# Kernel optimization log

Hardware: AMD Instinct MI355X
Metric: run time of the kernel (lower is better)

Reference implementation:

```python
import jax, jax.numpy as jnp
import numpy as np


def setup_inputs() -> dict:
    key = jax.random.key(0)
    ks = jax.random.split(key, 6)
    B, C, H, W = 4, 256, 64, 64
    C8 = C // 8
    s = 0.05
    return {
        "x": jax.random.normal(ks[0], (B, C, H, W), dtype=jnp.float32),
        "Wf": jax.random.normal(ks[1], (C8, C), dtype=jnp.float32) * s,
        "bf": jnp.zeros((C8,), dtype=jnp.float32),
        "Wg": jax.random.normal(ks[2], (C8, C), dtype=jnp.float32) * s,
        "bg": jnp.zeros((C8,), dtype=jnp.float32),
        "Wh": jax.random.normal(ks[3], (C, C), dtype=jnp.float32) * s,
        "bh": jnp.zeros((C,), dtype=jnp.float32),
        "gamma": jnp.ones((1,), dtype=jnp.float32),
    }


def reference(x, Wf, bf, Wg, bg, Wh, bh, gamma):
    B, C, H, W = x.shape
    N = H * W
    xf = x.reshape(B, C, N)  # [B, C, N] (1x1 conv == matmul over channels)
    f = jnp.einsum("kc,bcn->bkn", Wf, xf) + bf[None, :, None]  # [B, C/8, N]
    g = jnp.einsum("kc,bcn->bkn", Wg, xf) + bg[None, :, None]  # [B, C/8, N]
    h = jnp.einsum("oc,bcn->bon", Wh, xf) + bh[None, :, None]  # [B, C, N]
    # attention_map[b, n, m] = sum_k f[b,k,n] * g[b,k,m]  (f^T g)
    attn = jnp.einsum("bkn,bkm->bnm", f, g)  # [B, N, N]
    # softmax over dim -2 (the f-position axis), as in the torch module
    attn = jax.nn.softmax(attn, axis=-2)
    # out[b,c,m] = sum_n h[b,c,n] * attn[b,n,m]
    out = jnp.einsum("bcn,bnm->bcm", h, attn).reshape(B, C, H, W)
    return gamma * out + x
```

## Files before the change

kernel.cpp:

```cpp
#include <hip/hip_runtime.h>
#include <hip/hip_bf16.h>
#include <hip/hip_fp16.h>

typedef __attribute__((ext_vector_type(8))) short short8;
typedef __attribute__((ext_vector_type(8))) _Float16 half8;
typedef __attribute__((ext_vector_type(4))) float f32x4;
typedef unsigned short u16;
typedef unsigned int u32;

#define LOG2E 1.44269504088896f

__device__ __forceinline__ u16 f2bf(float f) {
  u32 u = __builtin_bit_cast(u32, f);
  u += 0x7fffu + ((u >> 16) & 1u);
  return (u16)(u >> 16);
}
__device__ __forceinline__ u16 f2h(float f) {
  _Float16 h = (_Float16)f;
  return __builtin_bit_cast(u16, h);
}

__global__ void k_prep(const float* __restrict__ x,
                       const float* __restrict__ Wf, const float* __restrict__ bfp,
                       const float* __restrict__ Wg, const float* __restrict__ bgp,
                       const float* __restrict__ Wh, const float* __restrict__ bhp,
                       u16* __restrict__ xT, u16* __restrict__ Wall,
                       float* __restrict__ ball)
{
  int bid = blockIdx.x, t = threadIdx.x;
  if (bid < 1024) {
    __shared__ u16 tile[64][68];
    int b = bid >> 8, c0 = ((bid >> 6) & 3) << 6, n0 = (bid & 63) << 6;
#pragma unroll
    for (int r = 0; r < 4; ++r) {
      int cl = (t >> 4) + r * 16, nl = (t & 15) * 4;
      const float4 v = *(const float4*)&x[(size_t)(b * 256 + c0 + cl) * 4096 + n0 + nl];
      tile[cl][nl + 0] = f2h(v.x); tile[cl][nl + 1] = f2h(v.y);
      tile[cl][nl + 2] = f2h(v.z); tile[cl][nl + 3] = f2h(v.w);
    }
    __syncthreads();
#pragma unroll
    for (int r = 0; r < 4; ++r) {
      int nl = (t >> 4) + r * 16, cl = (t & 15) * 4;
      ushort4 o;
      o.x = tile[cl + 0][nl]; o.y = tile[cl + 1][nl];
      o.z = tile[cl + 2][nl]; o.w = tile[cl + 3][nl];
      *(ushort4*)&xT[(size_t)(b * 4096 + n0 + nl) * 256 + c0 + cl] = o;
    }
  } else {
    int wb = bid - 1024;
    int e = wb * 1024 + t * 4;
    int r = e >> 8, c = e & 255;
    const float* src = (r < 32) ? (Wf + r * 256 + c)
                     : (r < 64) ? (Wg + (r - 32) * 256 + c)
                                : (Wh + (r - 64) * 256 + c);
    float4 v = *(const float4*)src;
    ushort4 o; o.x = f2h(v.x); o.y = f2h(v.y); o.z = f2h(v.z); o.w = f2h(v.w);
    *(ushort4*)&Wall[e] = o;
    if (wb == 0 && t < 80) {
#pragma unroll
      for (int i = 0; i < 4; ++i) {
        int idx = t * 4 + i;
        ball[idx] = (idx < 32) ? bfp[idx] : (idx < 64) ? bgp[idx - 32] : bhp[idx - 64];
      }
    }
  }
}

__global__ __launch_bounds__(256, 4)
void k_proj(const u16* __restrict__ xT, const u16* __restrict__ Wall,
            const float* __restrict__ ball,
            u16* __restrict__ q, u16* __restrict__ kmat, u16* __restrict__ hbf)
{
  int bid = blockIdx.x, t = threadIdx.x;
  int w = t >> 6, l = t & 63, lg = l >> 4, li = l & 15;
  f32x4 Z = {0.f, 0.f, 0.f, 0.f};
  if (bid < 256) {
    int b = bid >> 6, n0 = (bid & 63) << 6;
    int rbase = w * 16;
    half8 aw[8];
#pragma unroll
    for (int kk = 0; kk < 8; ++kk)
      aw[kk] = *(const half8*)&Wall[(rbase + li) * 256 + kk * 32 + lg * 8];
    float bias[4];
#pragma unroll
    for (int j = 0; j < 4; ++j) bias[j] = ball[rbase + 4 * lg + j];
#pragma unroll
    for (int nn = 0; nn < 4; ++nn) {
      int n = n0 + nn * 16 + li;
      f32x4 acc = Z;
#pragma unroll
      for (int kk = 0; kk < 8; ++kk) {
        half8 bx = *(const half8*)&xT[(size_t)(b * 4096 + n) * 256 + kk * 32 + lg * 8];
        acc = __builtin_amdgcn_mfma_f32_16x16x32_f16(aw[kk], bx, acc, 0, 0, 0);
      }
      ushort4 o;
      o.x = f2h(acc[0] + bias[0]); o.y = f2h(acc[1] + bias[1]);
      o.z = f2h(acc[2] + bias[2]); o.w = f2h(acc[3] + bias[3]);
      u16* dst = (rbase < 32)
               ? (kmat + (size_t)(b * 4096 + n) * 32 + rbase + 4 * lg)
               : (q    + (size_t)(b * 4096 + n) * 32 + (rbase - 32) + 4 * lg);
      *(ushort4*)dst = o;
    }
  } else {
    int hb = bid - 256;
    int b = hb >> 8, rt = (hb >> 6) & 3, n0 = (hb & 63) << 6;
    int r0 = 64 + rt * 64;
    int nbase = n0 + w * 16;
    half8 ax[8];
#pragma unroll
    for (int kk = 0; kk < 8; ++kk)
      ax[kk] = *(const half8*)&xT[(size_t)(b * 4096 + nbase + li) * 256 + kk * 32 + lg * 8];
#pragma unroll
    for (int rr = 0; rr < 4; ++rr) {
      int r = r0 + rr * 16 + li;
      f32x4 acc = Z;
#pragma unroll
      for (int kk = 0; kk < 8; ++kk) {
        half8 bw = *(const half8*)&Wall[r * 256 + kk * 32 + lg * 8];
        acc = __builtin_amdgcn_mfma_f32_16x16x32_f16(ax[kk], bw, acc, 0, 0, 0);
      }
      float bias = ball[r];
      ushort4 o;
      o.x = f2bf(acc[0] + bias); o.y = f2bf(acc[1] + bias);
      o.z = f2bf(acc[2] + bias); o.w = f2bf(acc[3] + bias);
      *(ushort4*)&hbf[(size_t)(b * 256 + r - 64) * 4096 + nbase + 4 * lg] = o;
    }
  }
}

__global__ __launch_bounds__(512, 2)
void k_attn(const u16* __restrict__ q, const u16* __restrict__ kmat,
            const u16* __restrict__ hbf, const float* __restrict__ xin,
            const float* __restrict__ gam, float* __restrict__ out)
{
  __shared__ __align__(16) u16 Pl[64 * 64];
  __shared__ float mrg[2 * 4096];
  __shared__ float sums[64];

  int bid = blockIdx.x, t = threadIdx.x;
  int b = (bid >> 1) & 3;
  int mt = ((bid >> 3) << 1) | (bid & 1);
  int m0 = mt << 6;
  int w = t >> 6, l = t & 63, lg = l >> 4, li = l & 15;
  int msub = w & 3, nh = w >> 2;
  int csub = msub,  kh = nh;

  const u16* qb = q    + (size_t)b * 4096 * 32;
  const u16* kb = kmat + (size_t)b * 4096 * 32;
  const u16* hb = hbf  + (size_t)b * 256 * 4096;

  half8 aQ = *(const half8*)&qb[(m0 + msub * 16 + li) * 32 + lg * 8];

  f32x4 Z = {0.f, 0.f, 0.f, 0.f};
  f32x4 acc[4][4];
#pragma unroll
  for (int mi = 0; mi < 4; ++mi)
#pragma unroll
    for (int ci = 0; ci < 4; ++ci) acc[mi][ci] = Z;
  float vsum[4] = {0.f, 0.f, 0.f, 0.f};

  half8 kf0 = *(const half8*)&kb[((nh * 2 + 0) * 16 + li) * 32 + lg * 8];
  half8 kf1 = *(const half8*)&kb[((nh * 2 + 1) * 16 + li) * 32 + lg * 8];
  short8 vb[4];
#pragma unroll
  for (int ff = 0; ff < 4; ++ff)
    vb[ff] = *(const short8*)&hb[(size_t)(csub * 64 + ff * 16 + li) * 4096 + kh * 32 + lg * 8];

  for (int it = 0; it < 64; ++it) {
    int n0 = it * 64;
    int n1 = (n0 + 64) & 4095;

    f32x4 s0 = __builtin_amdgcn_mfma_f32_16x16x32_f16(aQ, kf0, Z, 0, 0, 0);
    f32x4 s1 = __builtin_amdgcn_mfma_f32_16x16x32_f16(aQ, kf1, Z, 0, 0, 0);

    kf0 = *(const half8*)&kb[(n1 + (nh * 2 + 0) * 16 + li) * 32 + lg * 8];
    kf1 = *(const half8*)&kb[(n1 + (nh * 2 + 1) * 16 + li) * 32 + lg * 8];

    u16 pu[8];
#pragma unroll
    for (int j = 0; j < 4; ++j) {
      float p0 = exp2f(s0[j] * LOG2E);
      float p1 = exp2f(s1[j] * LOG2E);
      vsum[j] += p0 + p1;
      pu[j]     = f2bf(p0);
      pu[4 + j] = f2bf(p1);
    }

    asm volatile("s_waitcnt lgkmcnt(0)" ::: "memory");
    __builtin_amdgcn_s_barrier();

#pragma unroll
    for (int s = 0; s < 2; ++s) {
      int nc = (nh * 2 + s) * 16 + li;
#pragma unroll
      for (int j = 0; j < 4; ++j) {
        int m = msub * 16 + 4 * lg + j;
        Pl[m * 64 + (((nc >> 3) ^ (m & 7)) << 3) + (nc & 7)] = pu[s * 4 + j];
      }
    }

    asm volatile("s_waitcnt lgkmcnt(0)" ::: "memory");
    __builtin_amdgcn_s_barrier();

    short8 pa[4];
#pragma unroll
    for (int mi = 0; mi < 4; ++mi) {
      int m = mi * 16 + li;
      int blk = (kh * 4 + lg) ^ (m & 7);
      pa[mi] = *(const short8*)&Pl[m * 64 + blk * 8];
    }
#pragma unroll
    for (int mi = 0; mi < 4; ++mi)
#pragma unroll
      for (int ci = 0; ci < 4; ++ci)
        acc[mi][ci] = __builtin_amdgcn_mfma_f32_16x16x32_bf16(pa[mi], vb[ci], acc[mi][ci], 0, 0, 0);

#pragma unroll
    for (int ff = 0; ff < 4; ++ff)
      vb[ff] = *(const short8*)&hb[(size_t)(csub * 64 + ff * 16 + li) * 4096 + n1 + kh * 32 + lg * 8];
  }

#pragma unroll
  for (int j = 0; j < 4; ++j) {
    float v = vsum[j];
    v += __shfl_xor(v, 1); v += __shfl_xor(v, 2);
    v += __shfl_xor(v, 4); v += __shfl_xor(v, 8);
    vsum[j] = v;
  }
  int mrow = msub * 16 + 4 * lg;
  if (nh == 0 && li == 0) {
#pragma unroll
    for (int j = 0; j < 4; ++j) sums[mrow + j] = vsum[j];
  }
  if (w == 4 || w == 5) {
#pragma unroll
    for (int mi = 0; mi < 4; ++mi)
#pragma unroll
      for (int ci = 0; ci < 4; ++ci)
#pragma unroll
        for (int j = 0; j < 4; ++j)
          mrg[(w - 4) * 4096 + (mi * 16 + ci * 4 + j) * 64 + l] = acc[mi][ci][j];
  }
  __syncthreads();
  if (nh == 1 && li == 0) {
#pragma unroll
    for (int j = 0; j < 4; ++j) sums[mrow + j] += vsum[j];
  }
  if (w == 0 || w == 1) {
#pragma unroll
    for (int mi = 0; mi < 4; ++mi)
#pragma unroll
      for (int ci = 0; ci < 4; ++ci)
#pragma unroll
        for (int j = 0; j < 4; ++j)
          acc[mi][ci][j] += mrg[w * 4096 + (mi * 16 + ci * 4 + j) * 64 + l];
  }
  __syncthreads();
  if (t < 64) sums[t] = 1.0f / sums[t];
  if (w == 6 || w == 7) {
#pragma unroll
    for (int mi = 0; mi < 4; ++mi)
#pragma unroll
      for (int ci = 0; ci < 4; ++ci)
#pragma unroll
        for (int j = 0; j < 4; ++j)
          mrg[(w - 6) * 4096 + (mi * 16 + ci * 4 + j) * 64 + l] = acc[mi][ci][j];
  }
  __syncthreads();
  if (w == 2 || w == 3) {
#pragma unroll
    for (int mi = 0; mi < 4; ++mi)
#pragma unroll
      for (int ci = 0; ci < 4; ++ci)
#pragma unroll
        for (int j = 0; j < 4; ++j)
          acc[mi][ci][j] += mrg[(w - 2) * 4096 + (mi * 16 + ci * 4 + j) * 64 + l];
  }
  if (w < 4) {
    float gamma = gam[0];
    float* ob = out + (size_t)b * 256 * 4096;
    const float* xb = xin + (size_t)b * 256 * 4096;
#pragma unroll
    for (int mi = 0; mi < 4; ++mi) {
      float inv[4];
#pragma unroll
      for (int j = 0; j < 4; ++j) inv[j] = sums[mi * 16 + 4 * lg + j];
#pragma unroll
      for (int ci = 0; ci < 4; ++ci) {
        int c = csub * 64 + ci * 16 + li;
        size_t base = (size_t)c * 4096 + m0 + mi * 16 + 4 * lg;
        float4 xv = *(const float4*)&xb[base];
        float4 ov;
        ov.x = gamma * acc[mi][ci][0] * inv[0] + xv.x;
        ov.y = gamma * acc[mi][ci][1] * inv[1] + xv.y;
        ov.z = gamma * acc[mi][ci][2] * inv[2] + xv.z;
        ov.w = gamma * acc[mi][ci][3] * inv[3] + xv.w;
        *(float4*)&ob[base] = ov;
      }
    }
  }
}

extern "C" void kernel_launch(void* const* d_in, const int* in_sizes, int n_in,
                              void* d_out, int out_size, void* d_ws, size_t ws_size,
                              hipStream_t stream)
{
  const float* x   = (const float*)d_in[0];
  const float* Wf  = (const float*)d_in[1];
  const float* bfp = (const float*)d_in[2];
  const float* Wg  = (const float*)d_in[3];
  const float* bgp = (const float*)d_in[4];
  const float* Wh  = (const float*)d_in[5];
  const float* bhp = (const float*)d_in[6];
  const float* gam = (const float*)d_in[7];
  float* out = (float*)d_out;

  char* ws = (char*)d_ws;
  u16*   xT   = (u16*)(ws);
  u16*   Wall = (u16*)(ws + 8388608);
  float* ball = (float*)(ws + 8552448);
  u16*   q    = (u16*)(ws + 8554496);
  u16*   km   = (u16*)(ws + 10651648);
  u16*   hbf  = (u16*)(ws + 12748800);

  k_prep<<<dim3(1104), dim3(256), 0, stream>>>(x, Wf, bfp, Wg, bgp, Wh, bhp, xT, Wall, ball);
  k_proj<<<dim3(1280), dim3(256), 0, stream>>>(xT, Wall, ball, q, km, hbf);
  k_attn<<<dim3(256),  dim3(512), 0, stream>>>(q, km, hbf, x, gam, out);
}
```

Before: 115.3 us.

## Restructure attention kernel with 32x32 MFMA, register-resident P and split-N warps

Rewrites the attention main loop to use 32x32x16 MFMAs, computing S transposed (K as A operand) so each lane's exp'd probabilities feed the PV MFMA directly from registers. This removes the LDS round-trip for P and one of the two barriers per iteration. Warps split the N range in halves with double-buffered K/V register prefetch and s_setprio around the MFMA block. The LOG2E scale is folded into the g weights and bias at prep time, and the final cross-warp reduction is simplified to a single swizzled LDS merge. Larger accumulators and double buffers raise register pressure, and the V loads become narrower 8-byte accesses.

```diff
diff --git a/kernel.cpp b/kernel.cpp
--- a/kernel.cpp
+++ b/kernel.cpp
@@ -5,6 +5,8 @@
 typedef __attribute__((ext_vector_type(8))) short short8;
 typedef __attribute__((ext_vector_type(8))) _Float16 half8;
 typedef __attribute__((ext_vector_type(4))) float f32x4;
+typedef __attribute__((ext_vector_type(16))) float f32x16;
+typedef __attribute__((ext_vector_type(4))) unsigned int uint4v;
 typedef unsigned short u16;
 typedef unsigned int u32;
 
@@ -18,6 +20,11 @@
 __device__ __forceinline__ u16 f2h(float f) {
   _Float16 h = (_Float16)f;
   return __builtin_bit_cast(u16, h);
+}
+__device__ __forceinline__ u32 cvtpk_bf16(float lo, float hi) {
+  u32 r;
+  asm("v_cvt_pk_bf16_f32 %0, %1, %2" : "=v"(r) : "v"(lo), "v"(hi));
+  return r;
 }
 
 __global__ void k_prep(const float* __restrict__ x,
@@ -50,18 +57,23 @@
   } else {
     int wb = bid - 1024;
     int e = wb * 1024 + t * 4;
-    int r = e >> 8, c = e & 255;
-    const float* src = (r < 32) ? (Wf + r * 256 + c)
-                     : (r < 64) ? (Wg + (r - 32) * 256 + c)
-                                : (Wh + (r - 64) * 256 + c);
+    int r = e >> 8;
+    const float* src = (r < 32) ? (Wf + e)
+                     : (r < 64) ? (Wg + e - 32 * 256)
+                                : (Wh + e - 64 * 256);
     float4 v = *(const float4*)src;
-    ushort4 o; o.x = f2h(v.x); o.y = f2h(v.y); o.z = f2h(v.z); o.w = f2h(v.w);
+    float sc = (r >= 32 && r < 64) ? LOG2E : 1.0f;
+    ushort4 o;
+    o.x = f2h(v.x * sc); o.y = f2h(v.y * sc);
+    o.z = f2h(v.z * sc); o.w = f2h(v.w * sc);
     *(ushort4*)&Wall[e] = o;
     if (wb == 0 && t < 80) {
 #pragma unroll
       for (int i = 0; i < 4; ++i) {
         int idx = t * 4 + i;
-        ball[idx] = (idx < 32) ? bfp[idx] : (idx < 64) ? bgp[idx - 32] : bhp[idx - 64];
+        ball[idx] = (idx < 32) ? bfp[idx]
+                  : (idx < 64) ? bgp[idx - 32] * LOG2E
+                               : bhp[idx - 64];
       }
     }
   }
@@ -134,168 +146,144 @@
             const u16* __restrict__ hbf, const float* __restrict__ xin,
             const float* __restrict__ gam, float* __restrict__ out)
 {
-  __shared__ __align__(16) u16 Pl[64 * 64];
-  __shared__ float mrg[2 * 4096];
-  __shared__ float sums[64];
+  __shared__ float accL[4 * 64 * 64];
+  __shared__ float vsL[64];
+  __shared__ float invL[64];
 
   int bid = blockIdx.x, t = threadIdx.x;
-  int b = (bid >> 1) & 3;
-  int mt = ((bid >> 3) << 1) | (bid & 1);
-  int m0 = mt << 6;
-  int w = t >> 6, l = t & 63, lg = l >> 4, li = l & 15;
-  int msub = w & 3, nh = w >> 2;
-  int csub = msub,  kh = nh;
-
-  const u16* qb = q    + (size_t)b * 4096 * 32;
+  int xcd = bid & 7;
+  int b = xcd >> 1;
+  int mg = ((xcd & 1) << 5) | (bid >> 3);
+  int m0 = mg << 6;
+  int w = t >> 6, l = t & 63, l31 = l & 31, hi = l >> 5;
+  int msub = w & 1, ch = (w >> 1) & 1, kh = w >> 2;
+  int mb = m0 + msub * 32;
+  int c0 = ch * 128;
+  int nbase = kh * 2048;
+
+  const u16* qb = q + (size_t)b * 4096 * 32;
   const u16* kb = kmat + (size_t)b * 4096 * 32;
-  const u16* hb = hbf  + (size_t)b * 256 * 4096;
-
-  half8 aQ = *(const half8*)&qb[(m0 + msub * 16 + li) * 32 + lg * 8];
-
-  f32x4 Z = {0.f, 0.f, 0.f, 0.f};
-  f32x4 acc[4][4];
-#pragma unroll
-  for (int mi = 0; mi < 4; ++mi)
-#pragma unroll
-    for (int ci = 0; ci < 4; ++ci) acc[mi][ci] = Z;
-  float vsum[4] = {0.f, 0.f, 0.f, 0.f};
-
-  half8 kf0 = *(const half8*)&kb[((nh * 2 + 0) * 16 + li) * 32 + lg * 8];
-  half8 kf1 = *(const half8*)&kb[((nh * 2 + 1) * 16 + li) * 32 + lg * 8];
-  short8 vb[4];
-#pragma unroll
-  for (int ff = 0; ff < 4; ++ff)
-    vb[ff] = *(const short8*)&hb[(size_t)(csub * 64 + ff * 16 + li) * 4096 + kh * 32 + lg * 8];
-
-  for (int it = 0; it < 64; ++it) {
-    int n0 = it * 64;
-    int n1 = (n0 + 64) & 4095;
-
-    f32x4 s0 = __builtin_amdgcn_mfma_f32_16x16x32_f16(aQ, kf0, Z, 0, 0, 0);
-    f32x4 s1 = __builtin_amdgcn_mfma_f32_16x16x32_f16(aQ, kf1, Z, 0, 0, 0);
-
-    kf0 = *(const half8*)&kb[(n1 + (nh * 2 + 0) * 16 + li) * 32 + lg * 8];
-    kf1 = *(const half8*)&kb[(n1 + (nh * 2 + 1) * 16 + li) * 32 + lg * 8];
-
-    u16 pu[8];
-#pragma unroll
-    for (int j = 0; j < 4; ++j) {
-      float p0 = exp2f(s0[j] * LOG2E);
-      float p1 = exp2f(s1[j] * LOG2E);
-      vsum[j] += p0 + p1;
-      pu[j]     = f2bf(p0);
-      pu[4 + j] = f2bf(p1);
-    }
-
-    asm volatile("s_waitcnt lgkmcnt(0)" ::: "memory");
+  const u16* hb = hbf + (size_t)b * 256 * 4096;
+
+  half8 qf0 = *(const half8*)&qb[(mb + l31) * 32 + hi * 8];
+  half8 qf1 = *(const half8*)&qb[(mb + l31) * 32 + 16 + hi * 8];
+
+  f32x16 Z16 = {0,0,0,0,0,0,0,0,0,0,0,0,0,0,0,0};
+  f32x16 acc[4];
+#pragma unroll
+  for (int ct = 0; ct < 4; ++ct) acc[ct] = Z16;
+  float vsum = 0.f;
+
+  half8 kA0, kA1, kB0, kB1;
+  uint4v vA[4][2], vB[4][2];
+
+  auto loadK = [&](half8& k0, half8& k1, int n) {
+    k0 = *(const half8*)&kb[(n + l31) * 32 + hi * 8];
+    k1 = *(const half8*)&kb[(n + l31) * 32 + 16 + hi * 8];
+  };
+  auto loadV = [&](uint4v (&v)[4][2], int n) {
+#pragma unroll
+    for (int ct = 0; ct < 4; ++ct) {
+      const u16* rb = hb + (size_t)(c0 + ct * 32 + l31) * 4096 + n + 4 * hi;
+#pragma unroll
+      for (int kc = 0; kc < 2; ++kc) {
+        uint2 a = *(const uint2*)(rb + kc * 16);
+        uint2 bq = *(const uint2*)(rb + kc * 16 + 8);
+        uint4v vv = {a.x, a.y, bq.x, bq.y};
+        v[ct][kc] = vv;
+      }
+    }
+  };
+  auto step = [&](half8 k0, half8 k1, uint4v (&v)[4][2]) {
+    f32x16 sa = Z16;
+    sa = __builtin_amdgcn_mfma_f32_32x32x16_f16(k0, qf0, sa, 0, 0, 0);
+    sa = __builtin_amdgcn_mfma_f32_32x32x16_f16(k1, qf1, sa, 0, 0, 0);
+    float p[16];
+#pragma unroll
+    for (int r = 0; r < 16; ++r) p[r] = exp2f(sa[r]);
+    float s0 = 0.f, s1 = 0.f;
+#pragma unroll
+    for (int r = 0; r < 16; r += 2) { s0 += p[r]; s1 += p[r + 1]; }
+    vsum += s0 + s1;
+    u32 pk[8];
+#pragma unroll
+    for (int i = 0; i < 8; ++i) pk[i] = cvtpk_bf16(p[2 * i], p[2 * i + 1]);
+    uint4v a0 = {pk[0], pk[1], pk[2], pk[3]};
+    uint4v a1 = {pk[4], pk[5], pk[6], pk[7]};
+    short8 pa0 = __builtin_bit_cast(short8, a0);
+    short8 pa1 = __builtin_bit_cast(short8, a1);
+    __builtin_amdgcn_s_setprio(1);
+#pragma unroll
+    for (int ct = 0; ct < 4; ++ct) {
+      acc[ct] = __builtin_amdgcn_mfma_f32_32x32x16_bf16(
+          pa0, __builtin_bit_cast(short8, v[ct][0]), acc[ct], 0, 0, 0);
+      acc[ct] = __builtin_amdgcn_mfma_f32_32x32x16_bf16(
+          pa1, __builtin_bit_cast(short8, v[ct][1]), acc[ct], 0, 0, 0);
+    }
+    __builtin_amdgcn_s_setprio(0);
+  };
+
+  loadK(kA0, kA1, nbase);
+  loadV(vA, nbase);
+
+  for (int it = 0; it < 32; ++it) {
+    int nB = nbase + it * 64 + 32;
+    int nA2 = nbase + (((it + 1) * 64) & 2047);
     __builtin_amdgcn_s_barrier();
-
-#pragma unroll
-    for (int s = 0; s < 2; ++s) {
-      int nc = (nh * 2 + s) * 16 + li;
-#pragma unroll
-      for (int j = 0; j < 4; ++j) {
-        int m = msub * 16 + 4 * lg + j;
-        Pl[m * 64 + (((nc >> 3) ^ (m & 7)) << 3) + (nc & 7)] = pu[s * 4 + j];
-      }
-    }
-
-    asm volatile("s_waitcnt lgkmcnt(0)" ::: "memory");
-    __builtin_amdgcn_s_barrier();
-
-    short8 pa[4];
-#pragma unroll
-    for (int mi = 0; mi < 4; ++mi) {
-      int m = mi * 16 + li;
-      int blk = (kh * 4 + lg) ^ (m & 7);
-      pa[mi] = *(const short8*)&Pl[m * 64 + blk * 8];
-    }
-#pragma unroll
-    for (int mi = 0; mi < 4; ++mi)
-#pragma unroll
-      for (int ci = 0; ci < 4; ++ci)
-        acc[mi][ci] = __builtin_amdgcn_mfma_f32_16x16x32_bf16(pa[mi], vb[ci], acc[mi][ci], 0, 0, 0);
-
-#pragma unroll
-    for (int ff = 0; ff < 4; ++ff)
-      vb[ff] = *(const short8*)&hb[(size_t)(csub * 64 + ff * 16 + li) * 4096 + n1 + kh * 32 + lg * 8];
-  }
-
-#pragma unroll
-  for (int j = 0; j < 4; ++j) {
-    float v = vsum[j];
-    v += __shfl_xor(v, 1); v += __shfl_xor(v, 2);
-    v += __shfl_xor(v, 4); v += __shfl_xor(v, 8);
-    vsum[j] = v;
-  }
-  int mrow = msub * 16 + 4 * lg;
-  if (nh == 0 && li == 0) {
-#pragma unroll
-    for (int j = 0; j < 4; ++j) sums[mrow + j] = vsum[j];
-  }
-  if (w == 4 || w == 5) {
-#pragma unroll
-    for (int mi = 0; mi < 4; ++mi)
-#pragma unroll
-      for (int ci = 0; ci < 4; ++ci)
-#pragma unroll
-        for (int j = 0; j < 4; ++j)
-          mrg[(w - 4) * 4096 + (mi * 16 + ci * 4 + j) * 64 + l] = acc[mi][ci][j];
+    loadK(kB0, kB1, nB);
+    loadV(vB, nB);
+    step(kA0, kA1, vA);
+    loadK(kA0, kA1, nA2);
+    loadV(vA, nA2);
+    step(kB0, kB1, vB);
+  }
+
+  float vt = vsum + __shfl_xor(vsum, 32);
+  int region = w & 3;
+  if (kh == 1) {
+#pragma unroll
+    for (int ct = 0; ct < 4; ++ct)
+#pragma unroll
+      for (int g = 0; g < 4; ++g) {
+        int j4 = ct * 4 + g;
+        float4 v4 = {acc[ct][4 * g], acc[ct][4 * g + 1],
+                     acc[ct][4 * g + 2], acc[ct][4 * g + 3]};
+        *(float4*)&accL[region * 4096 + l * 64 + ((j4 ^ (l & 15)) * 4)] = v4;
+      }
+    if (ch == 0 && l < 32) vsL[msub * 32 + l31] = vt;
   }
   __syncthreads();
-  if (nh == 1 && li == 0) {
-#pragma unroll
-    for (int j = 0; j < 4; ++j) sums[mrow + j] += vsum[j];
-  }
-  if (w == 0 || w == 1) {
-#pragma unroll
-    for (int mi = 0; mi < 4; ++mi)
-#pragma unroll
-      for (int ci = 0; ci < 4; ++ci)
-#pragma unroll
-        for (int j = 0; j < 4; ++j)
-          acc[mi][ci][j] += mrg[w * 4096 + (mi * 16 + ci * 4 + j) * 64 + l];
+  if (kh == 0) {
+#pragma unroll
+    for (int ct = 0; ct < 4; ++ct)
+#pragma unroll
+      for (int g = 0; g < 4; ++g) {
+        int j4 = ct * 4 + g;
+        float4 v4 = *(const float4*)&accL[region * 4096 + l * 64 + ((j4 ^ (l & 15)) * 4)];
+        acc[ct][4 * g] += v4.x; acc[ct][4 * g + 1] += v4.y;
+        acc[ct][4 * g + 2] += v4.z; acc[ct][4 * g + 3] += v4.w;
+      }
+    if (ch == 0 && l < 32)
+      invL[msub * 32 + l31] = 1.0f / (vt + vsL[msub * 32 + l31]);
   }
   __syncthreads();
-  if (t < 64) sums[t] = 1.0f / sums[t];
-  if (w == 6 || w == 7) {
-#pragma unroll
-    for (int mi = 0; mi < 4; ++mi)
-#pragma unroll
-      for (int ci = 0; ci < 4; ++ci)
-#pragma unroll
-        for (int j = 0; j < 4; ++j)
-          mrg[(w - 6) * 4096 + (mi * 16 + ci * 4 + j) * 64 + l] = acc[mi][ci][j];
-  }
-  __syncthreads();
-  if (w == 2 || w == 3) {
-#pragma unroll
-    for (int mi = 0; mi < 4; ++mi)
-#pragma unroll
-      for (int ci = 0; ci < 4; ++ci)
-#pragma unroll
-        for (int j = 0; j < 4; ++j)
-          acc[mi][ci][j] += mrg[(w - 2) * 4096 + (mi * 16 + ci * 4 + j) * 64 + l];
-  }
-  if (w < 4) {
+  if (kh == 0) {
     float gamma = gam[0];
+    const float* xb = xin + (size_t)b * 256 * 4096;
     float* ob = out + (size_t)b * 256 * 4096;
-    const float* xb = xin + (size_t)b * 256 * 4096;
-#pragma unroll
-    for (int mi = 0; mi < 4; ++mi) {
-      float inv[4];
-#pragma unroll
-      for (int j = 0; j < 4; ++j) inv[j] = sums[mi * 16 + 4 * lg + j];
-#pragma unroll
-      for (int ci = 0; ci < 4; ++ci) {
-        int c = csub * 64 + ci * 16 + li;
-        size_t base = (size_t)c * 4096 + m0 + mi * 16 + 4 * lg;
+#pragma unroll
+    for (int g = 0; g < 4; ++g) {
+      float4 inv4 = *(const float4*)&invL[msub * 32 + 8 * g + 4 * hi];
+#pragma unroll
+      for (int ct = 0; ct < 4; ++ct) {
+        int c = c0 + ct * 32 + l31;
+        size_t base = (size_t)c * 4096 + mb + 8 * g + 4 * hi;
         float4 xv = *(const float4*)&xb[base];
         float4 ov;
-        ov.x = gamma * acc[mi][ci][0] * inv[0] + xv.x;
-        ov.y = gamma * acc[mi][ci][1] * inv[1] + xv.y;
-        ov.z = gamma * acc[mi][ci][2] * inv[2] + xv.z;
-        ov.w = gamma * acc[mi][ci][3] * inv[3] + xv.w;
+        ov.x = gamma * acc[ct][4 * g + 0] * inv4.x + xv.x;
+        ov.y = gamma * acc[ct][4 * g + 1] * inv4.y + xv.y;
+        ov.z = gamma * acc[ct][4 * g + 2] * inv4.z + xv.z;
+        ov.w = gamma * acc[ct][4 * g + 3] * inv4.w + xv.w;
         *(float4*)&ob[base] = ov;
       }
     }
```

Result: slower. 282.7 us (+145.2%).
